# Kernel tuning notes

Measured on AMD Instinct MI355X. Metric: run time of the kernel, lower is better.

The kernel has to match this reference:

```python
import jax, jax.numpy as jnp
import numpy as np

LSTM_SIZE = 512
MEM_SIZE = 2048
MEM_DIM = 256
NB_READS = 4
GAMMA = 0.95
EPS = 1e-8
B = 64
IN_RAW = 256
IN_TOTAL = IN_RAW + NB_READS * MEM_SIZE  # 8448
PARAM_DIM = (2 * MEM_DIM + 1) * NB_READS  # 2052


def setup_inputs() -> dict:
    key = jax.random.key(0)
    ks = jax.random.split(key, 8)
    s = 0.02
    return {
        "x": jax.random.normal(ks[0], (B, IN_RAW), jnp.float32),
        "M": jax.random.normal(ks[1], (B, MEM_SIZE, MEM_DIM), jnp.float32),
        "wu": jax.random.uniform(ks[2], (B, MEM_SIZE), jnp.float32),
        "wr": jax.random.uniform(ks[3], (B, NB_READS * MEM_SIZE), jnp.float32),
        "h0": jnp.zeros((LSTM_SIZE,), jnp.float32),
        "c0": jnp.zeros((LSTM_SIZE,), jnp.float32),
        "W_ih": jax.random.normal(ks[4], (4 * LSTM_SIZE, IN_TOTAL), jnp.float32) * s,
        "W_hh": jax.random.normal(ks[5], (4 * LSTM_SIZE, LSTM_SIZE), jnp.float32) * s,
        "b_ih": jnp.zeros((4 * LSTM_SIZE,), jnp.float32),
        "b_hh": jnp.zeros((4 * LSTM_SIZE,), jnp.float32),
        "W_p": jax.random.normal(ks[6], (PARAM_DIM, LSTM_SIZE), jnp.float32) * s,
        "b_p": jax.random.uniform(ks[7], (PARAM_DIM,), jnp.float32, -0.1, 0.1),
    }


def _lstm_scan(x_seq, h0, c0, W_ih, W_hh, b):
    # torch treats the 2-D input as an unbatched sequence of length B:
    # the recurrence runs across the batch axis with a single shared state.
    xW = x_seq @ W_ih.T + b  # [B, 4H] precomputed input contribution

    def step(carry, xw):
        h, c = carry
        g = xw + h @ W_hh.T
        i, f, gg, o = jnp.split(g, 4)
        c = jax.nn.sigmoid(f) * c + jax.nn.sigmoid(i) * jnp.tanh(gg)
        h = jax.nn.sigmoid(o) * jnp.tanh(c)
        return (h, c), h

    (hf, cf), hs = jax.lax.scan(step, (h0, c0), xW)
    return hs, hf, cf


def reference(x, M, wu, wr, h0, c0, W_ih, W_hh, b_ih, b_hh, W_p, b_p):
    ctrl_in = jnp.concatenate([x, wr], axis=-1)  # [B, IN_TOTAL]
    hs, hf, cf = _lstm_scan(ctrl_in, h0, c0, W_ih, W_hh, b_ih + b_hh)
    param = hs @ W_p.T + b_p  # [B, PARAM_DIM]

    nd = NB_READS * MEM_DIM
    k = jnp.tanh(param[:, :nd]).reshape(B, NB_READS, MEM_DIM)
    a = jnp.tanh(param[:, nd:2 * nd]).reshape(B, NB_READS, MEM_DIM)
    sig_alpha = jax.nn.sigmoid(param[:, -NB_READS:])  # [B, R]

    # least_used: topk(wu, k=MEM_SIZE) == full descending sort of indices
    order = jnp.argsort(-wu, axis=-1)  # [B, MEM_SIZE]
    lu_idx = order[:, -1]  # least used slot
    wlu = jax.nn.one_hot(order[:, -NB_READS:], MEM_SIZE, dtype=M.dtype).sum(1)  # [B, N]

    # read head addressing: cosine similarity softmax
    ip = jnp.einsum('brd,bnd->brn', k, M)  # [B, R, N]
    k_norm = jnp.sqrt(jnp.sum(k * k, -1))[:, :, None]
    M_norm = jnp.sqrt(jnp.sum(M * M, -1))[:, None, :]
    wr_t = jax.nn.softmax(ip / (k_norm * M_norm + EPS), axis=-1)  # [B, R, N]

    # write head addressing
    wr_prev3 = wr.reshape(B, NB_READS, MEM_SIZE)
    sa = sig_alpha[:, :, None]
    ww_t = sa * wr_prev3 + (1.0 - sa) * wlu[:, None, :]  # [B, R, N]

    wu_t = GAMMA * wu + wr_t.sum(1) + ww_t.sum(1)  # [B, N]

    erase = 1.0 - jax.nn.one_hot(lu_idx, MEM_SIZE, dtype=M.dtype)  # [B, N]
    M_t = M * erase[:, :, None] + jnp.einsum('brn,brd->bnd', ww_t, a)  # [B, N, D]
    r_t = jnp.einsum('brn,bnd->brd', wr_t, M_t).reshape(B, nd)  # [B, R*D]

    return jnp.concatenate([hs, r_t], axis=-1)  # [B, LSTM+R*D]
```

## Files before the change

kernel.cpp:

```cpp
#include <hip/hip_runtime.h>
#include <hip/hip_bf16.h>

#define BB 64
#define IN_RAW_ 256
#define KIN_ 8448
#define WRW 8192
#define PD_ 2052
#define XW_KS 16

__global__ __launch_bounds__(256) void k_xw_partial(
    const float* __restrict__ x, const float* __restrict__ wr,
    const float* __restrict__ Wih, float* __restrict__ xwp,
    float* __restrict__ zbuf) {
  if (blockIdx.x >= 512) {
    float4 z4 = make_float4(0.f, 0.f, 0.f, 0.f);
    float4* z = (float4*)zbuf;
    for (int i = (blockIdx.x - 512) * 256 + threadIdx.x; i < 82176; i += 40 * 256)
      z[i] = z4;
    return;
  }
  const int jb = blockIdx.x & 31;
  const int ks = blockIdx.x >> 5;
  const int j0 = jb << 6;
  const int k0 = (ks < 8) ? ks * 544 : 4352 + ((ks - 8) << 9);
  const int klen = (ks < 8) ? 544 : 512;
  __shared__ __align__(16) float As[32][68];
  __shared__ __align__(16) float Bs[32][68];
  const int tid = threadIdx.x;
  const int ti = tid & 15, tj = tid >> 4;
  const int lt = tid >> 2, lq = tid & 3;
  float acc[4][4];
#pragma unroll
  for (int i = 0; i < 4; ++i)
#pragma unroll
    for (int j = 0; j < 4; ++j) acc[i][j] = 0.f;
  for (int kc = 0; kc < klen; kc += 32) {
    __syncthreads();
    const int kb = k0 + kc + (lq << 3);
    float va[8], vb[8];
    if (kb < IN_RAW_) {
      const float* p = x + lt * IN_RAW_ + kb;
#pragma unroll
      for (int u = 0; u < 8; ++u) va[u] = p[u];
    } else {
      const float* p = wr + (size_t)lt * WRW + (kb - IN_RAW_);
#pragma unroll
      for (int u = 0; u < 8; ++u) va[u] = p[u];
    }
    {
      const float* p = Wih + (size_t)(j0 + lt) * KIN_ + kb;
#pragma unroll
      for (int u = 0; u < 8; ++u) vb[u] = p[u];
    }
#pragma unroll
    for (int u = 0; u < 8; ++u) As[(lq << 3) + u][lt] = va[u];
#pragma unroll
    for (int u = 0; u < 8; ++u) Bs[(lq << 3) + u][lt] = vb[u];
    __syncthreads();
#pragma unroll
    for (int kk = 0; kk < 32; ++kk) {
      const float4 a4 = *(const float4*)&As[kk][ti << 2];
      const float4 b4 = *(const float4*)&Bs[kk][tj << 2];
      const float av[4] = {a4.x, a4.y, a4.z, a4.w};
      const float bv[4] = {b4.x, b4.y, b4.z, b4.w};
#pragma unroll
      for (int i = 0; i < 4; ++i)
#pragma unroll
        for (int j = 0; j < 4; ++j) acc[i][j] = fmaf(av[i], bv[j], acc[i][j]);
    }
  }
#pragma unroll
  for (int i = 0; i < 4; ++i) {
    const int t = (ti << 2) + i;
    float* dst = xwp + (size_t)ks * 131072 + (t << 11) + j0 + (tj << 2);
    dst[0] = acc[i][0]; dst[1] = acc[i][1]; dst[2] = acc[i][2]; dst[3] = acc[i][3];
  }
}

__global__ __launch_bounds__(64, 1) void k_scan(
    const float* __restrict__ xwp, const float* __restrict__ bih,
    const float* __restrict__ bhh, const float* __restrict__ Whh,
    const float* __restrict__ h0, const float* __restrict__ c0,
    unsigned long long* __restrict__ ht, unsigned long long* __restrict__ xwt,
    float* __restrict__ out, const float* __restrict__ wu,
    int* __restrict__ t4) {
  const int W = blockIdx.x;
  const int l = threadIdx.x;
  if (W >= 192) {
    const int t = W - 192;
    for (int i = 0; i < 32; ++i) {
      const int col = (i << 6) + l;
      float s = bih[col] + bhh[col];
#pragma unroll
      for (int ks = 0; ks < XW_KS; ++ks)
        s += xwp[(size_t)ks * 131072 + (t << 11) + col];
      const unsigned long long pk =
          (1ull << 32) | (unsigned long long)__float_as_uint(s);
      __hip_atomic_store(xwt + (t << 11) + col, pk, __ATOMIC_RELAXED,
                         __HIP_MEMORY_SCOPE_AGENT);
    }
    return;
  }
  if (W >= 128) {
    const int b = W - 128;
    float val[32];
#pragma unroll
    for (int i = 0; i < 32; ++i) val[i] = wu[(b << 11) + (i << 6) + l];
    for (int pick = 0; pick < 4; ++pick) {
      float bv = 3.4e38f; int bi = -1;
#pragma unroll
      for (int i = 0; i < 32; ++i) {
        const int n = (i << 6) + l;
        const float v = val[i];
        if (v < bv || (v == bv && n > bi)) { bv = v; bi = n; }
      }
#pragma unroll
      for (int s = 1; s < 64; s <<= 1) {
        const float ov = __shfl_xor(bv, s);
        const int oi = __shfl_xor(bi, s);
        if (ov < bv || (ov == bv && oi > bi)) { bv = ov; bi = oi; }
      }
      if (l == 0) t4[(b << 2) + pick] = bi;
      if ((bi & 63) == l) val[bi >> 6] = 3.4e38f;
    }
    return;
  }
  const int d = l & 3;
  const int jj = (W << 2) + d;
  float wreg[16][8];
#pragma unroll
  for (int r = 0; r < 16; ++r) {
    const int row = ((r >> 2) << 9) + (W << 2) + (r & 3);
    const float* p = Whh + ((size_t)row << 9) + (l << 3);
#pragma unroll
    for (int u = 0; u < 8; ++u) wreg[r][u] = p[u];
  }
  float c = 0.f;
  if (l < 4) c = c0[jj];
  float h[8];
#pragma unroll
  for (int u = 0; u < 8; ++u) h[u] = h0[(l << 3) + u];

  for (int t = 0; t < 64; ++t) {
    float xv0 = 0, xv1 = 0, xv2 = 0, xv3 = 0;
    if (l < 4) {
      const unsigned long long* xp = xwt + (t << 11) + jj;
      unsigned long long x0, x1, x2, x3;
      for (;;) {
        x0 = __hip_atomic_load(xp, __ATOMIC_RELAXED, __HIP_MEMORY_SCOPE_AGENT);
        x1 = __hip_atomic_load(xp + 512, __ATOMIC_RELAXED, __HIP_MEMORY_SCOPE_AGENT);
        x2 = __hip_atomic_load(xp + 1024, __ATOMIC_RELAXED, __HIP_MEMORY_SCOPE_AGENT);
        x3 = __hip_atomic_load(xp + 1536, __ATOMIC_RELAXED, __HIP_MEMORY_SCOPE_AGENT);
        if ((unsigned)((x0 & x1 & x2 & x3) >> 32) == 1u) break;
      }
      xv0 = __uint_as_float((unsigned)x0);
      xv1 = __uint_as_float((unsigned)x1);
      xv2 = __uint_as_float((unsigned)x2);
      xv3 = __uint_as_float((unsigned)x3);
    }
    if (t > 0) {
      const unsigned long long* hp = ht + (t << 9) + (l << 3);
      unsigned long long va[8], vb[8];
#pragma unroll
      for (int u = 0; u < 8; ++u)
        va[u] = __hip_atomic_load(hp + u, __ATOMIC_RELAXED, __HIP_MEMORY_SCOPE_AGENT);
      for (;;) {
#pragma unroll
        for (int u = 0; u < 8; ++u)
          vb[u] = __hip_atomic_load(hp + u, __ATOMIC_RELAXED, __HIP_MEMORY_SCOPE_AGENT);
        bool ra = true;
#pragma unroll
        for (int u = 0; u < 8; ++u) ra &= ((unsigned)(va[u] >> 32) == (unsigned)t);
        if (ra) break;
#pragma unroll
        for (int u = 0; u < 8; ++u)
          va[u] = __hip_atomic_load(hp + u, __ATOMIC_RELAXED, __HIP_MEMORY_SCOPE_AGENT);
        bool rb_ = true;
#pragma unroll
        for (int u = 0; u < 8; ++u) rb_ &= ((unsigned)(vb[u] >> 32) == (unsigned)t);
        if (rb_) {
#pragma unroll
          for (int u = 0; u < 8; ++u) va[u] = vb[u];
          break;
        }
      }
#pragma unroll
      for (int u = 0; u < 8; ++u) h[u] = __uint_as_float((unsigned)va[u]);
    }
    float pr[16];
#pragma unroll
    for (int r = 0; r < 16; ++r) {
      float s = 0.f;
#pragma unroll
      for (int u = 0; u < 8; ++u) s = fmaf(wreg[r][u], h[u], s);
      pr[r] = s;
    }
    float v8[8], v4[4], v2[2], v1;
    {
      const bool b0 = (l & 1) != 0;
#pragma unroll
      for (int j = 0; j < 8; ++j) {
        const float keep = b0 ? pr[2 * j + 1] : pr[2 * j];
        const float send = b0 ? pr[2 * j] : pr[2 * j + 1];
        v8[j] = keep + __shfl_xor(send, 1);
      }
    }
    {
      const bool b1 = (l & 2) != 0;
#pragma unroll
      for (int j = 0; j < 4; ++j) {
        const float keep = b1 ? v8[2 * j + 1] : v8[2 * j];
        const float send = b1 ? v8[2 * j] : v8[2 * j + 1];
        v4[j] = keep + __shfl_xor(send, 2);
      }
    }
    {
      const bool b2 = (l & 4) != 0;
#pragma unroll
      for (int j = 0; j < 2; ++j) {
        const float keep = b2 ? v4[2 * j + 1] : v4[2 * j];
        const float send = b2 ? v4[2 * j] : v4[2 * j + 1];
        v2[j] = keep + __shfl_xor(send, 4);
      }
    }
    {
      const bool b3 = (l & 8) != 0;
      const float keep = b3 ? v2[1] : v2[0];
      const float send = b3 ? v2[0] : v2[1];
      v1 = keep + __shfl_xor(send, 8);
    }
    v1 += __shfl_xor(v1, 16);
    v1 += __shfl_xor(v1, 32);
    const float gi_ = __shfl(v1, d);
    const float gf_ = __shfl(v1, d + 4);
    const float gg_ = __shfl(v1, d + 8);
    const float go_ = __shfl(v1, d + 12);
    if (l < 4) {
      const float gi = gi_ + xv0;
      const float gf = gf_ + xv1;
      const float gg = gg_ + xv2;
      const float go = go_ + xv3;
      const float si = 1.f / (1.f + __expf(-gi));
      const float sf = 1.f / (1.f + __expf(-gf));
      const float so = 1.f / (1.f + __expf(-go));
      const float tg = 2.f / (1.f + __expf(-2.f * gg)) - 1.f;
      c = sf * c + si * tg;
      const float tc = 2.f / (1.f + __expf(-2.f * c)) - 1.f;
      const float hnew = so * tc;
      const unsigned long long pk =
          ((unsigned long long)(unsigned)(t + 1) << 32) |
          (unsigned long long)__float_as_uint(hnew);
      __hip_atomic_store(ht + ((t + 1) << 9) + jj, pk, __ATOMIC_RELAXED,
                         __HIP_MEMORY_SCOPE_AGENT);
      out[t * 1536 + jj] = hnew;
    }
  }
}

__global__ __launch_bounds__(256) void k_param(
    const float* __restrict__ outbuf, const float* __restrict__ Wp,
    const float* __restrict__ bp, float* __restrict__ km,
    float* __restrict__ am, float* __restrict__ sa) {
  const int j0 = blockIdx.x << 6;
  __shared__ __align__(16) float As[32][68];
  __shared__ __align__(16) float Bs[32][68];
  const int tid = threadIdx.x;
  const int ti = tid & 15, tj = tid >> 4;
  const int lt = tid >> 2, lq = tid & 3;
  float acc[4][4];
#pragma unroll
  for (int i = 0; i < 4; ++i)
#pragma unroll
    for (int j = 0; j < 4; ++j) acc[i][j] = 0.f;
  for (int kc = 0; kc < 512; kc += 32) {
    __syncthreads();
    const int kb = kc + (lq << 3);
    float va[8], vb[8];
    {
      const float* p = outbuf + lt * 1536 + kb;
#pragma unroll
      for (int u = 0; u < 8; ++u) va[u] = p[u];
    }
    const int brow = j0 + lt;
    if (brow < PD_) {
      const float* p = Wp + (size_t)brow * 512 + kb;
#pragma unroll
      for (int u = 0; u < 8; ++u) vb[u] = p[u];
    } else {
#pragma unroll
      for (int u = 0; u < 8; ++u) vb[u] = 0.f;
    }
#pragma unroll
    for (int u = 0; u < 8; ++u) As[(lq << 3) + u][lt] = va[u];
#pragma unroll
    for (int u = 0; u < 8; ++u) Bs[(lq << 3) + u][lt] = vb[u];
    __syncthreads();
#pragma unroll
    for (int kk = 0; kk < 32; ++kk) {
      const float4 a4 = *(const float4*)&As[kk][ti << 2];
      const float4 b4 = *(const float4*)&Bs[kk][tj << 2];
      const float av[4] = {a4.x, a4.y, a4.z, a4.w};
      const float bv[4] = {b4.x, b4.y, b4.z, b4.w};
#pragma unroll
      for (int i = 0; i < 4; ++i)
#pragma unroll
        for (int j = 0; j < 4; ++j) acc[i][j] = fmaf(av[i], bv[j], acc[i][j]);
    }
  }
#pragma unroll
  for (int i = 0; i < 4; ++i) {
    const int b = (ti << 2) + i;
#pragma unroll
    for (int j = 0; j < 4; ++j) {
      const int col = j0 + (tj << 2) + j;
      if (col < PD_) {
        const float v = acc[i][j] + bp[col];
        if (col < 1024) km[(b << 10) + col] = tanhf(v);
        else if (col < 2048) am[(b << 10) + col - 1024] = tanhf(v);
        else sa[(b << 2) + col - 2048] = 1.f / (1.f + expf(-v));
      }
    }
  }
}

__global__ __launch_bounds__(256) void k_ipv(
    const float* __restrict__ M, const float* __restrict__ km,
    const float* __restrict__ wr_in, const int* __restrict__ t4,
    float* __restrict__ pacc, float* __restrict__ pscal) {
  const int b = blockIdx.x >> 3;
  const int sl = blockIdx.x & 7;
  const int tid = threadIdx.x;
  const int wv = tid >> 6, l = tid & 63;
  const int g = l >> 4, j = l & 15;
  __shared__ float kns[4];
  __shared__ float t4eL[4][4];
  __shared__ __align__(16) float accW[4][4][256];
  __shared__ float SdW[4][4][4];
  __shared__ float ssW[4][4];
  if (tid < 16) t4eL[tid >> 2][tid & 3] = 0.f;
  {
    const float* kp = km + (((b << 2) + wv) << 8);
    float sq = 0.f;
#pragma unroll
    for (int i = 0; i < 4; ++i) { const float v = kp[l + (i << 6)]; sq = fmaf(v, v, sq); }
    sq += __shfl_xor(sq, 1);  sq += __shfl_xor(sq, 2);  sq += __shfl_xor(sq, 4);
    sq += __shfl_xor(sq, 8);  sq += __shfl_xor(sq, 16); sq += __shfl_xor(sq, 32);
    if (l == 0) kns[wv] = sqrtf(sq);
  }
  float kr[4][16];
#pragma unroll
  for (int r = 0; r < 4; ++r)
#pragma unroll
    for (int cc = 0; cc < 4; ++cc) {
      const float4 kv = *(const float4*)(km + (((b << 2) + r) << 8) + (cc << 6) + (j << 2));
      kr[r][(cc << 2) + 0] = kv.x; kr[r][(cc << 2) + 1] = kv.y;
      kr[r][(cc << 2) + 2] = kv.z; kr[r][(cc << 2) + 3] = kv.w;
    }
  int t4v[4];
#pragma unroll
  for (int ii = 0; ii < 4; ++ii) t4v[ii] = t4[(b << 2) + ii];
  __syncthreads();
  const float kn0 = kns[0], kn1 = kns[1], kn2 = kns[2], kn3 = kns[3];
  float aacc[4][16];
#pragma unroll
  for (int r = 0; r < 4; ++r)
#pragma unroll
    for (int k = 0; k < 16; ++k) aacc[r][k] = 0.f;
  float ssum[4] = {0.f, 0.f, 0.f, 0.f};
  float sdp[4] = {0.f, 0.f, 0.f, 0.f};
  for (int it = 0; it < 16; ++it) {
    const int n = (sl << 8) + (wv << 6) + (it << 2) + g;
    const float* mrow = M + (((size_t)b << 11) + n) * 256;
    float4 m4[4];
#pragma unroll
    for (int cc = 0; cc < 4; ++cc)
      m4[cc] = *(const float4*)(mrow + (cc << 6) + (j << 2));
    float s0 = 0.f, s1 = 0.f, s2 = 0.f, s3 = 0.f, sm = 0.f;
#pragma unroll
    for (int cc = 0; cc < 4; ++cc) {
      const float mv[4] = {m4[cc].x, m4[cc].y, m4[cc].z, m4[cc].w};
#pragma unroll
      for (int e = 0; e < 4; ++e) {
        sm = fmaf(mv[e], mv[e], sm);
        s0 = fmaf(kr[0][(cc << 2) + e], mv[e], s0);
        s1 = fmaf(kr[1][(cc << 2) + e], mv[e], s1);
        s2 = fmaf(kr[2][(cc << 2) + e], mv[e], s2);
        s3 = fmaf(kr[3][(cc << 2) + e], mv[e], s3);
      }
    }
    s0 += __shfl_xor(s0, 1); s0 += __shfl_xor(s0, 2); s0 += __shfl_xor(s0, 4); s0 += __shfl_xor(s0, 8);
    s1 += __shfl_xor(s1, 1); s1 += __shfl_xor(s1, 2); s1 += __shfl_xor(s1, 4); s1 += __shfl_xor(s1, 8);
    s2 += __shfl_xor(s2, 1); s2 += __shfl_xor(s2, 2); s2 += __shfl_xor(s2, 4); s2 += __shfl_xor(s2, 8);
    s3 += __shfl_xor(s3, 1); s3 += __shfl_xor(s3, 2); s3 += __shfl_xor(s3, 4); s3 += __shfl_xor(s3, 8);
    sm += __shfl_xor(sm, 1); sm += __shfl_xor(sm, 2); sm += __shfl_xor(sm, 4); sm += __shfl_xor(sm, 8);
    const float mnv = sqrtf(sm);
    float ev[4];
    ev[0] = __expf(s0 / fmaf(kn0, mnv, 1e-8f));
    ev[1] = __expf(s1 / fmaf(kn1, mnv, 1e-8f));
    ev[2] = __expf(s2 / fmaf(kn2, mnv, 1e-8f));
    ev[3] = __expf(s3 / fmaf(kn3, mnv, 1e-8f));
#pragma unroll
    for (int r = 0; r < 4; ++r) {
      ssum[r] += ev[r];
#pragma unroll
      for (int cc = 0; cc < 4; ++cc) {
        aacc[r][(cc << 2) + 0] = fmaf(ev[r], m4[cc].x, aacc[r][(cc << 2) + 0]);
        aacc[r][(cc << 2) + 1] = fmaf(ev[r], m4[cc].y, aacc[r][(cc << 2) + 1]);
        aacc[r][(cc << 2) + 2] = fmaf(ev[r], m4[cc].z, aacc[r][(cc << 2) + 2]);
        aacc[r][(cc << 2) + 3] = fmaf(ev[r], m4[cc].w, aacc[r][(cc << 2) + 3]);
      }
    }
    if (j < 4) {
      const float wq = wr_in[((size_t)b << 13) + (j << 11) + n];
#pragma unroll
      for (int r = 0; r < 4; ++r) sdp[r] = fmaf(ev[r], wq, sdp[r]);
    }
#pragma unroll
    for (int ii = 0; ii < 4; ++ii)
      if (n == t4v[ii] && j == 0) {
#pragma unroll
        for (int r = 0; r < 4; ++r) t4eL[ii][r] = ev[r];
      }
  }
#pragma unroll
  for (int r = 0; r < 4; ++r) {
    float v = ssum[r];
    v += __shfl_xor(v, 1);  v += __shfl_xor(v, 2);  v += __shfl_xor(v, 4);
    v += __shfl_xor(v, 8);  v += __shfl_xor(v, 16); v += __shfl_xor(v, 32);
    if (l == 0) ssW[wv][r] = v * 0.0625f;
    float sdv = sdp[r];
    sdv += __shfl_xor(sdv, 16);
    sdv += __shfl_xor(sdv, 32);
    if (l < 4) SdW[wv][l][r] = sdv;
  }
#pragma unroll
  for (int r = 0; r < 4; ++r)
#pragma unroll
    for (int k = 0; k < 16; ++k) {
      float v = aacc[r][k];
      v += __shfl_xor(v, 16);
      v += __shfl_xor(v, 32);
      aacc[r][k] = v;
    }
  if (l < 16) {
#pragma unroll
    for (int r = 0; r < 4; ++r)
#pragma unroll
      for (int cc = 0; cc < 4; ++cc)
#pragma unroll
        for (int ee = 0; ee < 4; ++ee)
          accW[wv][r][(cc << 6) + (l << 2) + ee] = aacc[r][(cc << 2) + ee];
  }
  __syncthreads();
  const int slice = (b << 3) + sl;
#pragma unroll
  for (int i = 0; i < 4; ++i) {
    const int e = tid + (i << 8);
    const float s4 = accW[0][i][tid] + accW[1][i][tid] + accW[2][i][tid] + accW[3][i][tid];
    pacc[((size_t)slice << 10) + e] = s4;
  }
  if (tid < 4)
    pscal[(slice << 6) + tid] = ssW[0][tid] + ssW[1][tid] + ssW[2][tid] + ssW[3][tid];
  if (tid < 16) {
    const int r = tid >> 2, q = tid & 3;
    pscal[(slice << 6) + 4 + (r << 2) + q] =
        SdW[0][q][r] + SdW[1][q][r] + SdW[2][q][r] + SdW[3][q][r];
    pscal[(slice << 6) + 20 + tid] = t4eL[tid >> 2][tid & 3];
  }
}

__global__ __launch_bounds__(256) void k_fin(
    const float* __restrict__ pacc, const float* __restrict__ pscal,
    const float* __restrict__ sa_g, const float* __restrict__ am,
    const float* __restrict__ M, const int* __restrict__ t4,
    float* __restrict__ out) {
  const int b = blockIdx.x;
  const int tid = threadIdx.x;
  __shared__ float Zs[4], Sl[16], wlu4[4], teL[4][4];
  if (tid < 4) {
    float z = 0.f;
    for (int sl = 0; sl < 8; ++sl) z += pscal[(((b << 3) + sl) << 6) + tid];
    Zs[tid] = z;
  }
  if (tid >= 16 && tid < 32) {
    const int ii = (tid - 16) >> 2, r = (tid - 16) & 3;
    float te = 0.f;
    for (int sl = 0; sl < 8; ++sl)
      te += pscal[(((b << 3) + sl) << 6) + 20 + (ii << 2) + r];
    teL[ii][r] = te;
  }
  __syncthreads();
  if (tid < 16) {
    const int r = tid >> 2, q = tid & 3;
    float sd = 0.f;
    for (int sl = 0; sl < 8; ++sl)
      sd += pscal[(((b << 3) + sl) << 6) + 4 + (r << 2) + q];
    const float Z = Zs[r];
    const float t4s = (teL[0][r] + teL[1][r] + teL[2][r] + teL[3][r]) / Z;
    const float sv = sa_g[(b << 2) + q];
    Sl[(r << 2) + q] = sv * (sd / Z) + (1.f - sv) * t4s;
    if (q == 0) wlu4[r] = teL[0][r] / Z;
  }
  __syncthreads();
  const int luv = t4[b << 2];
#pragma unroll
  for (int i = 0; i < 4; ++i) {
    const int e = tid + (i << 8);
    float s = 0.f;
    for (int sl = 0; sl < 8; ++sl)
      s += pacc[((size_t)(((b << 3) + sl)) << 10) + e];
    s /= Zs[i];
    s -= wlu4[i] * M[(((size_t)b << 11) + luv) * 256 + tid];
#pragma unroll
    for (int q = 0; q < 4; ++q)
      s = fmaf(Sl[(i << 2) + q], am[(((b << 2) + q) << 8) + tid], s);
    out[b * 1536 + 512 + e] = s;
  }
}

extern "C" void kernel_launch(void* const* d_in, const int* in_sizes, int n_in,
                              void* d_out, int out_size, void* d_ws, size_t ws_size,
                              hipStream_t stream) {
  (void)in_sizes; (void)n_in; (void)out_size;
  const float* x   = (const float*)d_in[0];
  const float* M   = (const float*)d_in[1];
  const float* wu  = (const float*)d_in[2];
  const float* wr  = (const float*)d_in[3];
  const float* h0  = (const float*)d_in[4];
  const float* c0  = (const float*)d_in[5];
  const float* Wih = (const float*)d_in[6];
  const float* Whh = (const float*)d_in[7];
  const float* bih = (const float*)d_in[8];
  const float* bhh = (const float*)d_in[9];
  const float* Wp  = (const float*)d_in[10];
  const float* bp  = (const float*)d_in[11];
  float* out = (float*)d_out;
  char* ws = (char*)d_ws;
  if (ws_size < 12457984u) return;

  float* xwp  = (float*)(ws + 0);
  float* km   = (float*)(ws + 8388608);
  float* am   = (float*)(ws + 8650752);
  float* sa   = (float*)(ws + 8912896);
  int*   t4   = (int*)(ws + 8913920);
  float* pacc = (float*)(ws + 8914944);
  float* pscal= (float*)(ws + 11012096);
  unsigned long long* ht  = (unsigned long long*)(ws + 11143168);
  unsigned long long* xwt = (unsigned long long*)(ws + 11409408);
  float* zbuf = (float*)(ws + 11143168);

  hipLaunchKernelGGL(k_xw_partial, dim3(552), dim3(256), 0, stream, x, wr, Wih, xwp, zbuf);
  hipLaunchKernelGGL(k_scan, dim3(256), dim3(64), 0, stream,
                     xwp, bih, bhh, Whh, h0, c0, ht, xwt, out, wu, t4);
  hipLaunchKernelGGL(k_param, dim3(33), dim3(256), 0, stream, out, Wp, bp, km, am, sa);
  hipLaunchKernelGGL(k_ipv, dim3(512), dim3(256), 0, stream, M, km, wr, t4, pacc, pscal);
  hipLaunchKernelGGL(k_fin, dim3(64), dim3(256), 0, stream,
                     pacc, pscal, sa, am, M, t4, out);
}
```

Measured before the change: 233.6 us.

## Overlap param projection with LSTM scan and fuse finalize into ipv

Removes the separate k_param kernel. 129 extra blocks are added to the scan kernel; each holds a 16-column slice of W_p in registers, waits on each step's tagged h, and writes km/am/sa as the recurrence runs. This hides the projection behind the serial scan. k_fin is folded into k_ipv: the last of the eight slice blocks per batch, found through an atomic counter zeroed by the existing zero-fill, does the final reduction, which saves a launch. The costs are extra polling traffic on h that may slow the critical scan path, and register pressure in the poller blocks.

```diff
diff --git a/kernel.cpp b/kernel.cpp
--- a/kernel.cpp
+++ b/kernel.cpp
@@ -15,7 +15,7 @@
   if (blockIdx.x >= 512) {
     float4 z4 = make_float4(0.f, 0.f, 0.f, 0.f);
     float4* z = (float4*)zbuf;
-    for (int i = (blockIdx.x - 512) * 256 + threadIdx.x; i < 82176; i += 40 * 256)
+    for (int i = (blockIdx.x - 512) * 256 + threadIdx.x; i < 82192; i += 40 * 256)
       z[i] = z4;
     return;
   }
@@ -83,9 +83,113 @@
     const float* __restrict__ h0, const float* __restrict__ c0,
     unsigned long long* __restrict__ ht, unsigned long long* __restrict__ xwt,
     float* __restrict__ out, const float* __restrict__ wu,
-    int* __restrict__ t4) {
+    int* __restrict__ t4, const float* __restrict__ Wp,
+    const float* __restrict__ bp, float* __restrict__ km,
+    float* __restrict__ am, float* __restrict__ sa) {
   const int W = blockIdx.x;
   const int l = threadIdx.x;
+  if (W >= 256) {
+    const int p = W - 256;
+    const int c0 = p << 4;
+    const int ncols = (c0 + 16 <= PD_) ? 16 : (PD_ - c0);
+    float wreg[16][8];
+#pragma unroll
+    for (int cI = 0; cI < 16; ++cI) {
+      if (cI < ncols) {
+        const float* wp = Wp + (size_t)(c0 + cI) * 512 + (l << 3);
+#pragma unroll
+        for (int u = 0; u < 8; ++u) wreg[cI][u] = wp[u];
+      } else {
+#pragma unroll
+        for (int u = 0; u < 8; ++u) wreg[cI][u] = 0.f;
+      }
+    }
+    float bpv = 0.f;
+    if (l < ncols) bpv = bp[c0 + l];
+    for (int t = 0; t < 64; ++t) {
+      const unsigned long long* hp = ht + ((t + 1) << 9) + (l << 3);
+      unsigned long long va[8], vb[8];
+      const unsigned tag = (unsigned)(t + 1);
+#pragma unroll
+      for (int u = 0; u < 8; ++u)
+        va[u] = __hip_atomic_load(hp + u, __ATOMIC_RELAXED, __HIP_MEMORY_SCOPE_AGENT);
+      for (;;) {
+#pragma unroll
+        for (int u = 0; u < 8; ++u)
+          vb[u] = __hip_atomic_load(hp + u, __ATOMIC_RELAXED, __HIP_MEMORY_SCOPE_AGENT);
+        bool ra = true;
+#pragma unroll
+        for (int u = 0; u < 8; ++u) ra &= ((unsigned)(va[u] >> 32) == tag);
+        if (ra) break;
+#pragma unroll
+        for (int u = 0; u < 8; ++u)
+          va[u] = __hip_atomic_load(hp + u, __ATOMIC_RELAXED, __HIP_MEMORY_SCOPE_AGENT);
+        bool rb_ = true;
+#pragma unroll
+        for (int u = 0; u < 8; ++u) rb_ &= ((unsigned)(vb[u] >> 32) == tag);
+        if (rb_) {
+#pragma unroll
+          for (int u = 0; u < 8; ++u) va[u] = vb[u];
+          break;
+        }
+      }
+      float h[8];
+#pragma unroll
+      for (int u = 0; u < 8; ++u) h[u] = __uint_as_float((unsigned)va[u]);
+      float pr[16];
+#pragma unroll
+      for (int r = 0; r < 16; ++r) {
+        float s = 0.f;
+#pragma unroll
+        for (int u = 0; u < 8; ++u) s = fmaf(wreg[r][u], h[u], s);
+        pr[r] = s;
+      }
+      float v8[8], v4[4], v2[2], v1;
+      {
+        const bool b0 = (l & 1) != 0;
+#pragma unroll
+        for (int j = 0; j < 8; ++j) {
+          const float keep = b0 ? pr[2 * j + 1] : pr[2 * j];
+          const float send = b0 ? pr[2 * j] : pr[2 * j + 1];
+          v8[j] = keep + __shfl_xor(send, 1);
+        }
+      }
+      {
+        const bool b1 = (l & 2) != 0;
+#pragma unroll
+        for (int j = 0; j < 4; ++j) {
+          const float keep = b1 ? v8[2 * j + 1] : v8[2 * j];
+          const float send = b1 ? v8[2 * j] : v8[2 * j + 1];
+          v4[j] = keep + __shfl_xor(send, 2);
+        }
+      }
+      {
+        const bool b2 = (l & 4) != 0;
+#pragma unroll
+        for (int j = 0; j < 2; ++j) {
+          const float keep = b2 ? v4[2 * j + 1] : v4[2 * j];
+          const float send = b2 ? v4[2 * j] : v4[2 * j + 1];
+          v2[j] = keep + __shfl_xor(send, 4);
+        }
+      }
+      {
+        const bool b3 = (l & 8) != 0;
+        const float keep = b3 ? v2[1] : v2[0];
+        const float send = b3 ? v2[0] : v2[1];
+        v1 = keep + __shfl_xor(send, 8);
+      }
+      v1 += __shfl_xor(v1, 16);
+      v1 += __shfl_xor(v1, 32);
+      if (l < ncols) {
+        const float v = v1 + bpv;
+        const int col = c0 + l;
+        if (col < 1024) km[(t << 10) + col] = tanhf(v);
+        else if (col < 2048) am[(t << 10) + col - 1024] = tanhf(v);
+        else sa[(t << 2) + col - 2048] = 1.f / (1.f + expf(-v));
+      }
+    }
+    return;
+  }
   if (W >= 192) {
     const int t = W - 192;
     for (int i = 0; i < 32; ++i) {
@@ -257,76 +361,12 @@
   }
 }
 
-__global__ __launch_bounds__(256) void k_param(
-    const float* __restrict__ outbuf, const float* __restrict__ Wp,
-    const float* __restrict__ bp, float* __restrict__ km,
-    float* __restrict__ am, float* __restrict__ sa) {
-  const int j0 = blockIdx.x << 6;
-  __shared__ __align__(16) float As[32][68];
-  __shared__ __align__(16) float Bs[32][68];
-  const int tid = threadIdx.x;
-  const int ti = tid & 15, tj = tid >> 4;
-  const int lt = tid >> 2, lq = tid & 3;
-  float acc[4][4];
-#pragma unroll
-  for (int i = 0; i < 4; ++i)
-#pragma unroll
-    for (int j = 0; j < 4; ++j) acc[i][j] = 0.f;
-  for (int kc = 0; kc < 512; kc += 32) {
-    __syncthreads();
-    const int kb = kc + (lq << 3);
-    float va[8], vb[8];
-    {
-      const float* p = outbuf + lt * 1536 + kb;
-#pragma unroll
-      for (int u = 0; u < 8; ++u) va[u] = p[u];
-    }
-    const int brow = j0 + lt;
-    if (brow < PD_) {
-      const float* p = Wp + (size_t)brow * 512 + kb;
-#pragma unroll
-      for (int u = 0; u < 8; ++u) vb[u] = p[u];
-    } else {
-#pragma unroll
-      for (int u = 0; u < 8; ++u) vb[u] = 0.f;
-    }
-#pragma unroll
-    for (int u = 0; u < 8; ++u) As[(lq << 3) + u][lt] = va[u];
-#pragma unroll
-    for (int u = 0; u < 8; ++u) Bs[(lq << 3) + u][lt] = vb[u];
-    __syncthreads();
-#pragma unroll
-    for (int kk = 0; kk < 32; ++kk) {
-      const float4 a4 = *(const float4*)&As[kk][ti << 2];
-      const float4 b4 = *(const float4*)&Bs[kk][tj << 2];
-      const float av[4] = {a4.x, a4.y, a4.z, a4.w};
-      const float bv[4] = {b4.x, b4.y, b4.z, b4.w};
-#pragma unroll
-      for (int i = 0; i < 4; ++i)
-#pragma unroll
-        for (int j = 0; j < 4; ++j) acc[i][j] = fmaf(av[i], bv[j], acc[i][j]);
-    }
-  }
-#pragma unroll
-  for (int i = 0; i < 4; ++i) {
-    const int b = (ti << 2) + i;
-#pragma unroll
-    for (int j = 0; j < 4; ++j) {
-      const int col = j0 + (tj << 2) + j;
-      if (col < PD_) {
-        const float v = acc[i][j] + bp[col];
-        if (col < 1024) km[(b << 10) + col] = tanhf(v);
-        else if (col < 2048) am[(b << 10) + col - 1024] = tanhf(v);
-        else sa[(b << 2) + col - 2048] = 1.f / (1.f + expf(-v));
-      }
-    }
-  }
-}
-
 __global__ __launch_bounds__(256) void k_ipv(
     const float* __restrict__ M, const float* __restrict__ km,
     const float* __restrict__ wr_in, const int* __restrict__ t4,
-    float* __restrict__ pacc, float* __restrict__ pscal) {
+    float* __restrict__ pacc, float* __restrict__ pscal,
+    unsigned int* __restrict__ cnt, const float* __restrict__ sa_g,
+    const float* __restrict__ am, float* __restrict__ out) {
   const int b = blockIdx.x >> 3;
   const int sl = blockIdx.x & 7;
   const int tid = threadIdx.x;
@@ -457,58 +497,65 @@
   for (int i = 0; i < 4; ++i) {
     const int e = tid + (i << 8);
     const float s4 = accW[0][i][tid] + accW[1][i][tid] + accW[2][i][tid] + accW[3][i][tid];
-    pacc[((size_t)slice << 10) + e] = s4;
+    __hip_atomic_store(&pacc[((size_t)slice << 10) + e], s4, __ATOMIC_RELAXED,
+                       __HIP_MEMORY_SCOPE_AGENT);
   }
   if (tid < 4)
-    pscal[(slice << 6) + tid] = ssW[0][tid] + ssW[1][tid] + ssW[2][tid] + ssW[3][tid];
+    __hip_atomic_store(&pscal[(slice << 6) + tid],
+                       ssW[0][tid] + ssW[1][tid] + ssW[2][tid] + ssW[3][tid],
+                       __ATOMIC_RELAXED, __HIP_MEMORY_SCOPE_AGENT);
   if (tid < 16) {
     const int r = tid >> 2, q = tid & 3;
-    pscal[(slice << 6) + 4 + (r << 2) + q] =
-        SdW[0][q][r] + SdW[1][q][r] + SdW[2][q][r] + SdW[3][q][r];
-    pscal[(slice << 6) + 20 + tid] = t4eL[tid >> 2][tid & 3];
-  }
-}
-
-__global__ __launch_bounds__(256) void k_fin(
-    const float* __restrict__ pacc, const float* __restrict__ pscal,
-    const float* __restrict__ sa_g, const float* __restrict__ am,
-    const float* __restrict__ M, const int* __restrict__ t4,
-    float* __restrict__ out) {
-  const int b = blockIdx.x;
-  const int tid = threadIdx.x;
-  __shared__ float Zs[4], Sl[16], wlu4[4], teL[4][4];
+    __hip_atomic_store(&pscal[(slice << 6) + 4 + (r << 2) + q],
+                       SdW[0][q][r] + SdW[1][q][r] + SdW[2][q][r] + SdW[3][q][r],
+                       __ATOMIC_RELAXED, __HIP_MEMORY_SCOPE_AGENT);
+    __hip_atomic_store(&pscal[(slice << 6) + 20 + tid], t4eL[tid >> 2][tid & 3],
+                       __ATOMIC_RELAXED, __HIP_MEMORY_SCOPE_AGENT);
+  }
+  __syncthreads();
+  __shared__ int lastF;
+  if (tid == 0) {
+    const unsigned old = __hip_atomic_fetch_add(&cnt[b], 1u, __ATOMIC_ACQ_REL,
+                                                __HIP_MEMORY_SCOPE_AGENT);
+    lastF = (old == 7u) ? 1 : 0;
+  }
+  __syncthreads();
+  if (!lastF) return;
+  __shared__ float Zs[4], Sl[16], wlu4[4], teF[4][4];
+#define PSC(i_) __hip_atomic_load(&pscal[i_], __ATOMIC_RELAXED, __HIP_MEMORY_SCOPE_AGENT)
   if (tid < 4) {
     float z = 0.f;
-    for (int sl = 0; sl < 8; ++sl) z += pscal[(((b << 3) + sl) << 6) + tid];
+    for (int s2 = 0; s2 < 8; ++s2) z += PSC((((b << 3) + s2) << 6) + tid);
     Zs[tid] = z;
   }
   if (tid >= 16 && tid < 32) {
     const int ii = (tid - 16) >> 2, r = (tid - 16) & 3;
     float te = 0.f;
-    for (int sl = 0; sl < 8; ++sl)
-      te += pscal[(((b << 3) + sl) << 6) + 20 + (ii << 2) + r];
-    teL[ii][r] = te;
+    for (int s2 = 0; s2 < 8; ++s2)
+      te += PSC((((b << 3) + s2) << 6) + 20 + (ii << 2) + r);
+    teF[ii][r] = te;
   }
   __syncthreads();
   if (tid < 16) {
     const int r = tid >> 2, q = tid & 3;
     float sd = 0.f;
-    for (int sl = 0; sl < 8; ++sl)
-      sd += pscal[(((b << 3) + sl) << 6) + 4 + (r << 2) + q];
+    for (int s2 = 0; s2 < 8; ++s2)
+      sd += PSC((((b << 3) + s2) << 6) + 4 + (r << 2) + q);
     const float Z = Zs[r];
-    const float t4s = (teL[0][r] + teL[1][r] + teL[2][r] + teL[3][r]) / Z;
+    const float t4s = (teF[0][r] + teF[1][r] + teF[2][r] + teF[3][r]) / Z;
     const float sv = sa_g[(b << 2) + q];
     Sl[(r << 2) + q] = sv * (sd / Z) + (1.f - sv) * t4s;
-    if (q == 0) wlu4[r] = teL[0][r] / Z;
+    if (q == 0) wlu4[r] = teF[0][r] / Z;
   }
   __syncthreads();
-  const int luv = t4[b << 2];
+  const int luv = t4v[0];
 #pragma unroll
   for (int i = 0; i < 4; ++i) {
     const int e = tid + (i << 8);
     float s = 0.f;
-    for (int sl = 0; sl < 8; ++sl)
-      s += pacc[((size_t)(((b << 3) + sl)) << 10) + e];
+    for (int s2 = 0; s2 < 8; ++s2)
+      s += __hip_atomic_load(&pacc[((size_t)(((b << 3) + s2)) << 10) + e],
+                             __ATOMIC_RELAXED, __HIP_MEMORY_SCOPE_AGENT);
     s /= Zs[i];
     s -= wlu4[i] * M[(((size_t)b << 11) + luv) * 256 + tid];
 #pragma unroll
@@ -516,6 +563,7 @@
       s = fmaf(Sl[(i << 2) + q], am[(((b << 2) + q) << 8) + tid], s);
     out[b * 1536 + 512 + e] = s;
   }
+#undef PSC
 }
 
 extern "C" void kernel_launch(void* const* d_in, const int* in_sizes, int n_in,
@@ -536,7 +584,7 @@
   const float* bp  = (const float*)d_in[11];
   float* out = (float*)d_out;
   char* ws = (char*)d_ws;
-  if (ws_size < 12457984u) return;
+  if (ws_size < 12458240u) return;
 
   float* xwp  = (float*)(ws + 0);
   float* km   = (float*)(ws + 8388608);
@@ -547,13 +595,13 @@
   float* pscal= (float*)(ws + 11012096);
   unsigned long long* ht  = (unsigned long long*)(ws + 11143168);
   unsigned long long* xwt = (unsigned long long*)(ws + 11409408);
+  unsigned int* cnt = (unsigned int*)(ws + 12457984);
   float* zbuf = (float*)(ws + 11143168);
 
   hipLaunchKernelGGL(k_xw_partial, dim3(552), dim3(256), 0, stream, x, wr, Wih, xwp, zbuf);
-  hipLaunchKernelGGL(k_scan, dim3(256), dim3(64), 0, stream,
-                     xwp, bih, bhh, Whh, h0, c0, ht, xwt, out, wu, t4);
-  hipLaunchKernelGGL(k_param, dim3(33), dim3(256), 0, stream, out, Wp, bp, km, am, sa);
-  hipLaunchKernelGGL(k_ipv, dim3(512), dim3(256), 0, stream, M, km, wr, t4, pacc, pscal);
-  hipLaunchKernelGGL(k_fin, dim3(64), dim3(256), 0, stream,
-                     pacc, pscal, sa, am, M, t4, out);
+  hipLaunchKernelGGL(k_scan, dim3(385), dim3(64), 0, stream,
+                     xwp, bih, bhh, Whh, h0, c0, ht, xwt, out, wu, t4,
+                     Wp, bp, km, am, sa);
+  hipLaunchKernelGGL(k_ipv, dim3(512), dim3(256), 0, stream,
+                     M, km, wr, t4, pacc, pscal, cnt, sa, am, out);
 }
```

New measurement: 336.8 us. 44.2% more time.
